# Optimization experiments

Hardware: AMD Instinct MI355X
Metric: run time of the kernel (lower is better)

The kernel has to match this reference:

```python
import jax, jax.numpy as jnp
import numpy as np


def setup_inputs() -> dict:
    key = jax.random.key(0)
    k1, k2, k3 = jax.random.split(key, 3)
    B, S, K, N = 4, 2048, 4096, 4096
    x = jax.random.normal(k1, (B, S, K), dtype=jnp.float32)
    # int8 weight table, symmetric range like post-quantization weights
    weight = jax.random.randint(k2, (N, K), -127, 128, dtype=jnp.int32).astype(jnp.int8)
    weight_scale = jnp.float32(0.01)
    bias = jax.random.normal(k3, (N,), dtype=jnp.float32)
    return {"x": x, "weight": weight, "weight_scale": weight_scale, "bias": bias}


def reference(x, weight, weight_scale, bias):
    # dynamic per-tensor activation quantization
    input_scale = jnp.max(jnp.abs(x)) / 127.0
    # torch float->int8 cast truncates toward zero; XLA convert does the same
    x_int8 = jnp.clip(x / input_scale, -127.0, 127.0).astype(jnp.int8)
    orig_shape = x.shape
    # int8 GEMM with int32 accumulation (torch._int_mm equivalent)
    out_int32 = jnp.matmul(
        x_int8.reshape(-1, orig_shape[-1]), weight.T,
        preferred_element_type=jnp.int32,
    )
    out = out_int32.astype(x.dtype) * (input_scale * weight_scale)
    out = out.reshape(*orig_shape[:-1], weight.shape[0])
    out = out + bias
    return out
```

## Files before the change

### kernel.cpp

```cpp
#include <hip/hip_runtime.h>
#include <stdint.h>

static constexpr int KD = 4096;
static constexpr int ND = 4096;
static constexpr int BK = 128;

using i32x4 = __attribute__((ext_vector_type(4))) int;

__device__ __forceinline__ void async_copy16(const void* g, void* l) {
    __builtin_amdgcn_global_load_lds(
        (const __attribute__((address_space(1))) void*)g,
        (__attribute__((address_space(3))) void*)l,
        16, 0, 0);
}

__device__ __forceinline__ uint32_t lds_addr(const void* p) {
    return (uint32_t)(uintptr_t)(__attribute__((address_space(3))) const void*)p;
}

template<int IMM>
__device__ __forceinline__ i32x4 dsr(uint32_t a) {
    i32x4 d;
    if constexpr (IMM == 0)
        asm volatile("ds_read_b128 %0, %1" : "=v"(d) : "v"(a));
    else
        asm volatile("ds_read_b128 %0, %1 offset:%2" : "=v"(d) : "v"(a), "n"(IMM));
    return d;
}

static constexpr int AB_BLOCKS = 2048;

__global__ __launch_bounds__(256) void prologue_kernel(
        const float* __restrict__ x, unsigned* __restrict__ out_bits, int n4,
        const int* __restrict__ w, int8_t* __restrict__ wq) {
    if (blockIdx.x < AB_BLOCKS) {
        int tid = blockIdx.x * blockDim.x + threadIdx.x;
        int stride = AB_BLOCKS * 256;
        const float4* x4 = (const float4*)x;
        float m0 = 0.f, m1 = 0.f, m2 = 0.f, m3 = 0.f;
        for (int i = tid; i < n4; i += 4 * stride) {
            float4 a = x4[i];
            float4 b = x4[i + stride];
            float4 c = x4[i + 2 * stride];
            float4 d = x4[i + 3 * stride];
            m0 = fmaxf(m0, fmaxf(fmaxf(fabsf(a.x), fabsf(a.y)),
                                 fmaxf(fabsf(a.z), fabsf(a.w))));
            m1 = fmaxf(m1, fmaxf(fmaxf(fabsf(b.x), fabsf(b.y)),
                                 fmaxf(fabsf(b.z), fabsf(b.w))));
            m2 = fmaxf(m2, fmaxf(fmaxf(fabsf(c.x), fabsf(c.y)),
                                 fmaxf(fabsf(c.z), fabsf(c.w))));
            m3 = fmaxf(m3, fmaxf(fmaxf(fabsf(d.x), fabsf(d.y)),
                                 fmaxf(fabsf(d.z), fabsf(d.w))));
        }
        float m = fmaxf(fmaxf(m0, m1), fmaxf(m2, m3));
        #pragma unroll
        for (int off = 32; off > 0; off >>= 1)
            m = fmaxf(m, __shfl_down(m, off, 64));
        __shared__ float wmax[4];
        int lane = threadIdx.x & 63, wv = threadIdx.x >> 6;
        if (lane == 0) wmax[wv] = m;
        __syncthreads();
        if (threadIdx.x == 0) {
            float b = fmaxf(fmaxf(wmax[0], wmax[1]), fmaxf(wmax[2], wmax[3]));
            atomicMax(out_bits, __float_as_uint(b));
        }
    } else {
        int t = (blockIdx.x - AB_BLOCKS) * 256 + threadIdx.x;
        const int4* w4 = (const int4*)(w) + (size_t)t * 4;
        int4 packed;
        int* pp = (int*)&packed;
        #pragma unroll
        for (int g = 0; g < 4; ++g) {
            int4 v = w4[g];
            pp[g] = (v.x & 255) | ((v.y & 255) << 8) |
                    ((v.z & 255) << 16) | (v.w << 24);
        }
        ((int4*)wq)[t] = packed;
    }
}

__global__ __launch_bounds__(256) void quant_x_kernel(
        const float* __restrict__ x, const unsigned* __restrict__ mx_bits,
        int8_t* __restrict__ xq) {
    int tid = blockIdx.x * blockDim.x + threadIdx.x;
    float s = __uint_as_float(*mx_bits) / 127.0f;
    float4 v = ((const float4*)x)[tid];
    float t0 = fminf(127.f, fmaxf(-127.f, v.x / s));
    float t1 = fminf(127.f, fmaxf(-127.f, v.y / s));
    float t2 = fminf(127.f, fmaxf(-127.f, v.z / s));
    float t3 = fminf(127.f, fmaxf(-127.f, v.w / s));
    int q0 = (int)t0, q1 = (int)t1, q2 = (int)t2, q3 = (int)t3;
    ((int*)xq)[tid] = (q0 & 255) | ((q1 & 255) << 8) |
                      ((q2 & 255) << 16) | (q3 << 24);
}

__global__ __launch_bounds__(512, 2) void gemm_i8_kernel(
        const int8_t* __restrict__ Aq,
        const int8_t* __restrict__ Wq,
        const unsigned* __restrict__ mx_bits,
        const float* __restrict__ wscale_p,
        const float* __restrict__ bias,
        float* __restrict__ out) {
    __shared__ __align__(16) int8_t lds_a[2][32768];
    __shared__ __align__(16) int8_t lds_b[2][32768];

    const int fid = blockIdx.y * gridDim.x + blockIdx.x;
    const int swz = (fid & 7) * 64 + (fid >> 3);
    const int bx = swz & 15;
    const int by = swz >> 4;

    const int tid  = threadIdx.x;
    const int lane = tid & 63;
    const int w    = tid >> 6;
    const int wm = (w >> 2) * 128;
    const int wn = (w & 3) * 64;
    const int fr = lane & 15;
    const int kc = lane >> 4;

    const int r   = tid >> 3;
    const int gch = (tid & 7) ^ (r & 7);
    const int8_t* agp[2][2];
    const int8_t* bgp[2][2];
    #pragma unroll
    for (int s = 0; s < 2; ++s)
        #pragma unroll
        for (int c2 = 0; c2 < 2; ++c2) {
            agp[s][c2] = Aq + (size_t)(by * 256 + r + s * 64 + c2 * 128) * KD
                            + gch * 16;
            bgp[s][c2] = Wq + (size_t)(bx * 256 + r + s * 128 + c2 * 64) * KD
                            + gch * 16;
        }

    const uint32_t Abase = lds_addr(&lds_a[0][0]);
    const uint32_t Bbase = lds_addr(&lds_b[0][0]);
    uint32_t aofs[8];
    #pragma unroll
    for (int i = 0; i < 8; ++i) {
        int row = wm + i * 16 + fr;
        int s   = (row >> 6) & 1;
        int sr  = (row & 63) | ((row & 128) >> 1);
        aofs[i] = Abase + s * 16384 + sr * 128 + ((kc ^ (sr & 7)) << 4);
    }
    uint32_t bofs[4];
    #pragma unroll
    for (int j = 0; j < 4; ++j) {
        int row = wn + j * 16 + fr;
        int s   = row >> 7;
        int sr  = row & 127;
        bofs[j] = Bbase + s * 16384 + sr * 128 + ((kc ^ (sr & 7)) << 4);
    }

    i32x4 acc[8][4] = {};
    i32x4 bf[4][2];
    i32x4 af[2][2];

#define STG_A(kb, par, s) do { \
    async_copy16(agp[s][0] + (kb), &lds_a[par][(s) * 16384 + tid * 16]); \
    async_copy16(agp[s][1] + (kb), &lds_a[par][(s) * 16384 + tid * 16 + 8192]); \
} while (0)
#define STG_B(kb, par, s) do { \
    async_copy16(bgp[s][0] + (kb), &lds_b[par][(s) * 16384 + tid * 16]); \
    async_copy16(bgp[s][1] + (kb), &lds_b[par][(s) * 16384 + tid * 16 + 8192]); \
} while (0)
#define STG_B2A(kb, par) do { STG_B(kb, par, 1); STG_A(kb, par, 0); } while (0)
#define NOPS ((void)0)
#define VMW6 asm volatile("s_waitcnt vmcnt(6)" ::: "memory")
#define VMW0 asm volatile("s_waitcnt vmcnt(0)" ::: "memory")

#define PHASE(par, q, STAGE, TAIL) do { \
    if ((q) == 0) { \
        _Pragma("unroll") \
        for (int jj = 0; jj < 4; ++jj) { \
            bf[jj][0] = dsr<(par) * 32768>(bofs[jj]); \
            bf[jj][1] = dsr<(par) * 32768>(bofs[jj] ^ 64u); \
        } \
    } \
    af[0][0] = dsr<(par) * 32768>(aofs[2 * (q)]); \
    af[0][1] = dsr<(par) * 32768>(aofs[2 * (q)] ^ 64u); \
    af[1][0] = dsr<(par) * 32768>(aofs[2 * (q) + 1]); \
    af[1][1] = dsr<(par) * 32768>(aofs[2 * (q) + 1] ^ 64u); \
    STAGE; \
    __builtin_amdgcn_s_barrier(); \
    asm volatile("s_waitcnt lgkmcnt(0)" ::: "memory"); \
    __builtin_amdgcn_sched_barrier(0); \
    __builtin_amdgcn_s_setprio(1); \
    _Pragma("unroll") \
    for (int ss = 0; ss < 2; ++ss) \
        _Pragma("unroll") \
        for (int jj = 0; jj < 4; ++jj) \
            _Pragma("unroll") \
            for (int ii = 0; ii < 2; ++ii) \
                acc[2 * (q) + ii][jj] = __builtin_amdgcn_mfma_i32_16x16x64_i8( \
                    af[ii][ss], bf[jj][ss], acc[2 * (q) + ii][jj], 0, 0, 0); \
    __builtin_amdgcn_s_setprio(0); \
    TAIL; \
    __builtin_amdgcn_s_barrier(); \
} while (0)

#define TILE_STEADY(par, u) do { \
    const int kb1 = ((u) + 1) * BK; \
    const int kb2 = ((u) + 2) * BK; \
    PHASE(par, 0, STG_A(kb1, (par) ^ 1, 1), NOPS); \
    PHASE(par, 1, STG_B(kb2, par, 0), NOPS); \
    PHASE(par, 2, STG_B2A(kb2, par), NOPS); \
    PHASE(par, 3, NOPS, VMW6); \
} while (0)

    STG_A(0, 0, 0); STG_A(0, 0, 1); STG_B(0, 0, 0); STG_B(0, 0, 1);
    STG_B(BK, 1, 0); STG_B(BK, 1, 1); STG_A(BK, 1, 0);
    VMW6;
    __builtin_amdgcn_s_barrier();

    #pragma unroll 1
    for (int it = 0; it < 15; ++it) {
        const int u0 = 2 * it;
        TILE_STEADY(0, u0);
        TILE_STEADY(1, u0 + 1);
    }

    PHASE(0, 0, STG_A(31 * BK, 1, 1), NOPS);
    PHASE(0, 1, NOPS, NOPS);
    PHASE(0, 2, NOPS, NOPS);
    PHASE(0, 3, NOPS, VMW0);
    PHASE(1, 0, NOPS, NOPS);
    PHASE(1, 1, NOPS, NOPS);
    PHASE(1, 2, NOPS, NOPS);
    PHASE(1, 3, NOPS, NOPS);

    const float stot = (__uint_as_float(*mx_bits) / 127.0f) * (*wscale_p);
    float bj[4];
    #pragma unroll
    for (int j = 0; j < 4; ++j)
        bj[j] = bias[bx * 256 + wn + j * 16 + fr];

    #pragma unroll
    for (int i = 0; i < 8; ++i) {
        int mrow = by * 256 + wm + i * 16 + kc * 4;
        #pragma unroll
        for (int rr = 0; rr < 4; ++rr) {
            float* orow = out + (size_t)(mrow + rr) * ND + bx * 256;
            #pragma unroll
            for (int j = 0; j < 4; ++j)
                orow[wn + j * 16 + fr] = (float)acc[i][j][rr] * stot + bj[j];
        }
    }
}

extern "C" void kernel_launch(void* const* d_in, const int* in_sizes, int n_in,
                              void* d_out, int out_size, void* d_ws, size_t ws_size,
                              hipStream_t stream) {
    const float* x      = (const float*)d_in[0];
    const int*   wgt    = (const int*)d_in[1];
    const float* wscale = (const float*)d_in[2];
    const float* bias   = (const float*)d_in[3];
    float* out = (float*)d_out;

    const int M = in_sizes[0] / KD;

    uint8_t* ws = (uint8_t*)d_ws;
    unsigned* mx_bits = (unsigned*)ws;
    int8_t* xq = (int8_t*)(ws + 256);
    int8_t* wq = (int8_t*)(ws + 256 + (size_t)M * KD);

    const int pk_blocks = (ND * KD / 16) / 256;
    hipMemsetAsync(mx_bits, 0, 4, stream);
    prologue_kernel<<<AB_BLOCKS + pk_blocks, 256, 0, stream>>>(
        x, mx_bits, (M * KD) / 4, wgt, wq);
    quant_x_kernel<<<(M * KD / 4) / 256, 256, 0, stream>>>(x, mx_bits, xq);
    gemm_i8_kernel<<<dim3(ND / 256, M / 256), 512, 0, stream>>>(
        xq, wq, mx_bits, wscale, bias, out);
}
```

Before: 408.7 us.

## Double-buffer A fragments across phases and grid-stride the quantize kernel

```diff
diff --git a/kernel.cpp b/kernel.cpp
--- a/kernel.cpp
+++ b/kernel.cpp
@@ -81,17 +81,29 @@
 
 __global__ __launch_bounds__(256) void quant_x_kernel(
         const float* __restrict__ x, const unsigned* __restrict__ mx_bits,
-        int8_t* __restrict__ xq) {
-    int tid = blockIdx.x * blockDim.x + threadIdx.x;
-    float s = __uint_as_float(*mx_bits) / 127.0f;
-    float4 v = ((const float4*)x)[tid];
-    float t0 = fminf(127.f, fmaxf(-127.f, v.x / s));
-    float t1 = fminf(127.f, fmaxf(-127.f, v.y / s));
-    float t2 = fminf(127.f, fmaxf(-127.f, v.z / s));
-    float t3 = fminf(127.f, fmaxf(-127.f, v.w / s));
-    int q0 = (int)t0, q1 = (int)t1, q2 = (int)t2, q3 = (int)t3;
-    ((int*)xq)[tid] = (q0 & 255) | ((q1 & 255) << 8) |
-                      ((q2 & 255) << 16) | (q3 << 24);
+        int8_t* __restrict__ xq, int n4) {
+    const int tid = blockIdx.x * blockDim.x + threadIdx.x;
+    const int stride = AB_BLOCKS * 256;
+    const float s = __uint_as_float(*mx_bits) / 127.0f;
+    const float4* x4 = (const float4*)x;
+    int* q4 = (int*)xq;
+    for (int i = tid; i < n4; i += 4 * stride) {
+        float4 v0 = x4[i];
+        float4 v1 = x4[i + stride];
+        float4 v2 = x4[i + 2 * stride];
+        float4 v3 = x4[i + 3 * stride];
+        #pragma unroll
+        for (int g = 0; g < 4; ++g) {
+            float4 v = g == 0 ? v0 : g == 1 ? v1 : g == 2 ? v2 : v3;
+            float t0 = fminf(127.f, fmaxf(-127.f, v.x / s));
+            float t1 = fminf(127.f, fmaxf(-127.f, v.y / s));
+            float t2 = fminf(127.f, fmaxf(-127.f, v.z / s));
+            float t3 = fminf(127.f, fmaxf(-127.f, v.w / s));
+            int q0 = (int)t0, q1 = (int)t1, q2 = (int)t2, q3 = (int)t3;
+            q4[i + g * stride] = (q0 & 255) | ((q1 & 255) << 8) |
+                                 ((q2 & 255) << 16) | (q3 << 24);
+        }
+    }
 }
 
 __global__ __launch_bounds__(512, 2) void gemm_i8_kernel(
@@ -152,7 +164,8 @@
 
     i32x4 acc[8][4] = {};
     i32x4 bf[4][2];
-    i32x4 af[2][2];
+    i32x4 afX[2][2];
+    i32x4 afY[2][2];
 
 #define STG_A(kb, par, s) do { \
     async_copy16(agp[s][0] + (kb), &lds_a[par][(s) * 16384 + tid * 16]); \
@@ -164,68 +177,106 @@
 } while (0)
 #define STG_B2A(kb, par) do { STG_B(kb, par, 1); STG_A(kb, par, 0); } while (0)
 #define NOPS ((void)0)
-#define VMW6 asm volatile("s_waitcnt vmcnt(6)" ::: "memory")
-#define VMW0 asm volatile("s_waitcnt vmcnt(0)" ::: "memory")
-
-#define PHASE(par, q, STAGE, TAIL) do { \
-    if ((q) == 0) { \
-        _Pragma("unroll") \
-        for (int jj = 0; jj < 4; ++jj) { \
-            bf[jj][0] = dsr<(par) * 32768>(bofs[jj]); \
-            bf[jj][1] = dsr<(par) * 32768>(bofs[jj] ^ 64u); \
-        } \
+#define VMW(N) asm volatile("s_waitcnt vmcnt(" #N ")" ::: "memory")
+#define LGKM(N) do { \
+    asm volatile("s_waitcnt lgkmcnt(" #N ")" ::: "memory"); \
+    __builtin_amdgcn_sched_barrier(0); \
+} while (0)
+#define BAR __builtin_amdgcn_s_barrier()
+
+#define RD_AF(DST, I0, PAR) do { \
+    DST[0][0] = dsr<(PAR) * 32768>(aofs[I0]); \
+    DST[0][1] = dsr<(PAR) * 32768>(aofs[I0] ^ 64u); \
+    DST[1][0] = dsr<(PAR) * 32768>(aofs[(I0) + 1]); \
+    DST[1][1] = dsr<(PAR) * 32768>(aofs[(I0) + 1] ^ 64u); \
+} while (0)
+#define RD_BF(PAR) do { \
+    bf[0][0] = dsr<(PAR) * 32768>(bofs[0]); \
+    bf[1][0] = dsr<(PAR) * 32768>(bofs[1]); \
+    bf[2][0] = dsr<(PAR) * 32768>(bofs[2]); \
+    bf[3][0] = dsr<(PAR) * 32768>(bofs[3]); \
+    bf[0][1] = dsr<(PAR) * 32768>(bofs[0] ^ 64u); \
+    bf[1][1] = dsr<(PAR) * 32768>(bofs[1] ^ 64u); \
+    bf[2][1] = dsr<(PAR) * 32768>(bofs[2] ^ 64u); \
+    bf[3][1] = dsr<(PAR) * 32768>(bofs[3] ^ 64u); \
+} while (0)
+
+#define MFMA8(Q, AF, SS) do { \
+    _Pragma("unroll") \
+    for (int jj = 0; jj < 4; ++jj) { \
+        acc[2 * (Q)][jj] = __builtin_amdgcn_mfma_i32_16x16x64_i8( \
+            AF[0][SS], bf[jj][SS], acc[2 * (Q)][jj], 0, 0, 0); \
+        acc[2 * (Q) + 1][jj] = __builtin_amdgcn_mfma_i32_16x16x64_i8( \
+            AF[1][SS], bf[jj][SS], acc[2 * (Q) + 1][jj], 0, 0, 0); \
     } \
-    af[0][0] = dsr<(par) * 32768>(aofs[2 * (q)]); \
-    af[0][1] = dsr<(par) * 32768>(aofs[2 * (q)] ^ 64u); \
-    af[1][0] = dsr<(par) * 32768>(aofs[2 * (q) + 1]); \
-    af[1][1] = dsr<(par) * 32768>(aofs[2 * (q) + 1] ^ 64u); \
-    STAGE; \
-    __builtin_amdgcn_s_barrier(); \
-    asm volatile("s_waitcnt lgkmcnt(0)" ::: "memory"); \
-    __builtin_amdgcn_sched_barrier(0); \
+} while (0)
+
+#define PHASE0(P, AFC, AFN, STG, TAILVM) do { \
+    STG; \
+    RD_BF(P); \
+    RD_AF(AFN, 2, P); \
+    LGKM(8); \
     __builtin_amdgcn_s_setprio(1); \
-    _Pragma("unroll") \
-    for (int ss = 0; ss < 2; ++ss) \
-        _Pragma("unroll") \
-        for (int jj = 0; jj < 4; ++jj) \
-            _Pragma("unroll") \
-            for (int ii = 0; ii < 2; ++ii) \
-                acc[2 * (q) + ii][jj] = __builtin_amdgcn_mfma_i32_16x16x64_i8( \
-                    af[ii][ss], bf[jj][ss], acc[2 * (q) + ii][jj], 0, 0, 0); \
+    MFMA8(0, AFC, 0); \
+    LGKM(4); \
+    MFMA8(0, AFC, 1); \
     __builtin_amdgcn_s_setprio(0); \
-    TAIL; \
-    __builtin_amdgcn_s_barrier(); \
-} while (0)
-
-#define TILE_STEADY(par, u) do { \
-    const int kb1 = ((u) + 1) * BK; \
-    const int kb2 = ((u) + 2) * BK; \
-    PHASE(par, 0, STG_A(kb1, (par) ^ 1, 1), NOPS); \
-    PHASE(par, 1, STG_B(kb2, par, 0), NOPS); \
-    PHASE(par, 2, STG_B2A(kb2, par), NOPS); \
-    PHASE(par, 3, NOPS, VMW6); \
+    TAILVM; \
+    BAR; \
+} while (0)
+
+#define PHASEQ(Q, AFC, AFN, NI0, NPAR, STG, TAILVM) do { \
+    STG; \
+    RD_AF(AFN, NI0, NPAR); \
+    LGKM(4); \
+    __builtin_amdgcn_s_setprio(1); \
+    MFMA8(Q, AFC, 0); \
+    MFMA8(Q, AFC, 1); \
+    __builtin_amdgcn_s_setprio(0); \
+    TAILVM; \
+    BAR; \
+} while (0)
+
+#define TILE_P0(kb1, kb2) do { \
+    PHASE0(0, afX, afY, STG_A(kb1, 1, 1), VMW(6)); \
+    PHASEQ(1, afY, afX, 4, 0, STG_B(kb2, 0, 0), VMW(4)); \
+    PHASEQ(2, afX, afY, 6, 0, STG_B2A(kb2, 0), VMW(6)); \
+    PHASEQ(3, afY, afX, 0, 1, NOPS, NOPS); \
+} while (0)
+#define TILE_P1(kb1, kb2) do { \
+    PHASE0(1, afX, afY, STG_A(kb1, 0, 1), VMW(6)); \
+    PHASEQ(1, afY, afX, 4, 1, STG_B(kb2, 1, 0), VMW(4)); \
+    PHASEQ(2, afX, afY, 6, 1, STG_B2A(kb2, 1), VMW(6)); \
+    PHASEQ(3, afY, afX, 0, 0, NOPS, NOPS); \
 } while (0)
 
     STG_A(0, 0, 0); STG_A(0, 0, 1); STG_B(0, 0, 0); STG_B(0, 0, 1);
     STG_B(BK, 1, 0); STG_B(BK, 1, 1); STG_A(BK, 1, 0);
-    VMW6;
-    __builtin_amdgcn_s_barrier();
+    VMW(6);
+    BAR;
+    RD_AF(afX, 0, 0);
 
     #pragma unroll 1
     for (int it = 0; it < 15; ++it) {
         const int u0 = 2 * it;
-        TILE_STEADY(0, u0);
-        TILE_STEADY(1, u0 + 1);
-    }
-
-    PHASE(0, 0, STG_A(31 * BK, 1, 1), NOPS);
-    PHASE(0, 1, NOPS, NOPS);
-    PHASE(0, 2, NOPS, NOPS);
-    PHASE(0, 3, NOPS, VMW0);
-    PHASE(1, 0, NOPS, NOPS);
-    PHASE(1, 1, NOPS, NOPS);
-    PHASE(1, 2, NOPS, NOPS);
-    PHASE(1, 3, NOPS, NOPS);
+        TILE_P0((u0 + 1) * BK, (u0 + 2) * BK);
+        TILE_P1((u0 + 2) * BK, (u0 + 3) * BK);
+    }
+
+    PHASE0(0, afX, afY, STG_A(31 * BK, 1, 1), VMW(6));
+    PHASEQ(1, afY, afX, 4, 0, NOPS, VMW(2));
+    PHASEQ(2, afX, afY, 6, 0, NOPS, VMW(0));
+    PHASEQ(3, afY, afX, 0, 1, NOPS, NOPS);
+    PHASE0(1, afX, afY, NOPS, NOPS);
+    PHASEQ(1, afY, afX, 4, 1, NOPS, NOPS);
+    PHASEQ(2, afX, afY, 6, 1, NOPS, NOPS);
+    {
+        LGKM(0);
+        __builtin_amdgcn_s_setprio(1);
+        MFMA8(3, afY, 0);
+        MFMA8(3, afY, 1);
+        __builtin_amdgcn_s_setprio(0);
+    }
 
     const float stot = (__uint_as_float(*mx_bits) / 127.0f) * (*wscale_p);
     float bj[4];
@@ -266,7 +317,8 @@
     hipMemsetAsync(mx_bits, 0, 4, stream);
     prologue_kernel<<<AB_BLOCKS + pk_blocks, 256, 0, stream>>>(
         x, mx_bits, (M * KD) / 4, wgt, wq);
-    quant_x_kernel<<<(M * KD / 4) / 256, 256, 0, stream>>>(x, mx_bits, xq);
+    quant_x_kernel<<<AB_BLOCKS, 256, 0, stream>>>(
+        x, mx_bits, xq, (M * KD) / 4);
     gemm_i8_kernel<<<dim3(ND / 256, M / 256), 512, 0, stream>>>(
         xq, wq, mx_bits, wscale, bias, out);
 }
```

New measurement: 407.7 us. About the same (-0.2%).
